# Kernel tuning notes

Hardware: AMD Instinct MI355X
Metric: run time of the kernel (lower is better)

The kernel has to match this reference:

```python
import jax, jax.numpy as jnp
import numpy as np
import math

# ---------- real Wigner 3j (Clebsch-Gordan in real spherical-harmonic basis) ----------

def _w3j_complex(l1, l2, l3):
    F = math.factorial
    tri = F(l1 + l2 - l3) * F(l1 - l2 + l3) * F(-l1 + l2 + l3) / F(l1 + l2 + l3 + 1)
    C = np.zeros((2 * l1 + 1, 2 * l2 + 1, 2 * l3 + 1))
    for m1 in range(-l1, l1 + 1):
        for m2 in range(-l2, l2 + 1):
            m3 = -m1 - m2
            if abs(m3) > l3:
                continue
            pref = (-1.0) ** (l1 - l2 - m3) * math.sqrt(
                tri * F(l1 + m1) * F(l1 - m1) * F(l2 + m2) * F(l2 - m2) * F(l3 + m3) * F(l3 - m3))
            s = 0.0
            for t in range(max(0, l2 - l3 - m1, l1 - l3 + m2),
                           min(l1 + l2 - l3, l1 - m1, l2 + m2) + 1):
                s += (-1.0) ** t / (F(t) * F(l1 + l2 - l3 - t) * F(l1 - m1 - t)
                                    * F(l2 + m2 - t) * F(l3 - l2 + m1 + t) * F(l3 - l1 - m2 + t))
            C[m1 + l1, m2 + l2, m3 + l3] = pref * s
    return C

def _U_real(l):
    # complex -> real spherical harmonic change of basis, rows indexed by real m in [-l, l]
    U = np.zeros((2 * l + 1, 2 * l + 1), dtype=complex)
    U[l, l] = 1.0
    s2 = 1.0 / math.sqrt(2.0)
    for m in range(1, l + 1):
        U[l + m, l + m] = (-1) ** m * s2
        U[l + m, l - m] = s2
        U[l - m, l - m] = 1j * s2
        U[l - m, l + m] = -1j * (-1) ** m * s2
    return U

def _w3j_real(l1, l2, l3):
    # 3j symbol is rotation invariant, so conjugating each index by U gives the real-basis 3j;
    # for even l1+l2+l3 (all paths here) the result is purely real. Frobenius norm is 1.
    Cc = _w3j_complex(l1, l2, l3)
    Cr = np.einsum('ia,jb,kc,abc->ijk', _U_real(l1), _U_real(l2), _U_real(l3), Cc)
    return np.ascontiguousarray(Cr.real.astype(np.float32))

_PATHS = [(4, 4), (4, 6), (6, 4), (6, 6)]  # CG-allowed couplings into 4e and into 6e
_CG = {(l1, l2, lo): jnp.asarray(_w3j_real(l1, l2, lo)) for lo in (4, 6) for (l1, l2) in _PATHS}
_A4 = math.sqrt(9.0 / 4.0)    # component normalization: sqrt(dim(4e) / n_paths)
_A6 = math.sqrt(13.0 / 4.0)   # component normalization: sqrt(dim(6e) / n_paths)
_K = 3                        # kernel_size
_COPIES = 4                   # upsample_factor**2


def setup_inputs() -> dict:
    key = jax.random.key(0)
    k1, k2, k3 = jax.random.split(key, 3)
    H = W = 768
    n = H * W
    return {
        'f4': jax.random.normal(k1, (n, 9), dtype=jnp.float32),
        'f6': jax.random.normal(k2, (n, 13), dtype=jnp.float32),
        'spatial_weights': jnp.ones((_K, _K), dtype=jnp.float32) / (_K * _K),
        'tp_weights': jax.random.normal(k3, (_COPIES, 8), dtype=jnp.float32),
        'H': H, 'W': W,
    }


def reference(f4, f6, spatial_weights, tp_weights, H, W):
    feats = jnp.concatenate([f4, f6], axis=-1)            # (HW, 22)
    Cch = feats.shape[-1]
    img = feats.reshape(H, W, Cch)
    pad = _K // 2
    img_p = jnp.pad(img, ((pad, pad), (pad, pad), (0, 0)), mode='edge')  # replicate padding
    # weighted 3x3 neighbor sum == depthwise conv with the shared spatial kernel
    kern = jnp.broadcast_to(spatial_weights[:, :, None, None], (_K, _K, 1, Cch)).astype(feats.dtype)
    nb = jax.lax.conv_general_dilated(
        img_p[None], kern, (1, 1), 'VALID',
        dimension_numbers=('NHWC', 'HWIO', 'NHWC'),
        feature_group_count=Cch)[0].reshape(-1, Cch)      # (HW, 22)

    x = {4: feats[:, :9], 6: feats[:, 9:]}                # center-pixel irreps
    y = {4: nb[:, :9], 6: nb[:, 9:]}                      # neighbor-aggregated irreps
    # path outputs are shared across copies; only the scalar path weights differ per copy
    t4 = jnp.stack([jnp.einsum('ijk,ni,nj->nk', _CG[(l1, l2, 4)], x[l1], y[l2]) for l1, l2 in _PATHS], 0)  # (4, HW, 9)
    t6 = jnp.stack([jnp.einsum('ijk,ni,nj->nk', _CG[(l1, l2, 6)], x[l1], y[l2]) for l1, l2 in _PATHS], 0)  # (4, HW, 13)
    out4 = _A4 * jnp.einsum('cp,pnk->nck', tp_weights[:, :4], t4)   # (HW, copies, 9)
    out6 = _A6 * jnp.einsum('cp,pnk->nck', tp_weights[:, 4:], t6)   # (HW, copies, 13)
    # per-copy [f4(9) | f6(13)] blocks concatenated along features, as in torch.cat(out_per_copy, -1)
    out = jnp.concatenate([out4, out6], axis=-1).reshape(-1, _COPIES * 22)  # (HW, 88)
    f4_size = 9 * _COPIES
    f4_out = out[:, :f4_size] + jnp.tile(f4, (1, _COPIES))   # matches torch's :36 slice + repeat residual
    f6_out = out[:, f4_size:] + jnp.tile(f6, (1, _COPIES))
    return f4_out, f6_out
```

## Files before the change

### kernel.cpp

```cpp
#include <hip/hip_runtime.h>
#include <utility>
#include <cstddef>

namespace cg {

struct FactTab { double f[24]; };
constexpr FactTab make_fact() {
  FactTab t{}; t.f[0] = 1.0;
  for (int i = 1; i < 24; ++i) t.f[i] = t.f[i-1] * (double)i;
  return t;
}
constexpr FactTab FT = make_fact();
constexpr double F(int n) { return FT.f[n]; }

constexpr double csqrt(double x) {
  if (x <= 0.0) return 0.0;
  double g = x > 1.0 ? x : 1.0;
  for (int i = 0; i < 200; ++i) {
    double ng = 0.5 * (g + x / g);
    if (ng >= g) break;
    g = ng;
  }
  return g;
}

struct T3 { double v[13][13][13]; };

constexpr T3 w3j_c(int l1, int l2, int l3) {
  T3 C{};
  const double tri = F(l1+l2-l3) * F(l1-l2+l3) * F(-l1+l2+l3) / F(l1+l2+l3+1);
  for (int m1 = -l1; m1 <= l1; ++m1) {
    for (int m2 = -l2; m2 <= l2; ++m2) {
      const int m3 = -m1 - m2;
      if (m3 < -l3 || m3 > l3) continue;
      const int e = l1 - l2 - m3;
      const double sign = (((e % 2) + 2) % 2) ? -1.0 : 1.0;
      const double pref = sign * csqrt(tri * F(l1+m1) * F(l1-m1) * F(l2+m2)
                                           * F(l2-m2) * F(l3+m3) * F(l3-m3));
      int t0 = 0;
      if (l2 - l3 - m1 > t0) t0 = l2 - l3 - m1;
      if (l1 - l3 + m2 > t0) t0 = l1 - l3 + m2;
      int t1 = l1 + l2 - l3;
      if (l1 - m1 < t1) t1 = l1 - m1;
      if (l2 + m2 < t1) t1 = l2 + m2;
      double s = 0.0;
      for (int t = t0; t <= t1; ++t) {
        const double term = 1.0 / (F(t) * F(l1+l2-l3-t) * F(l1-m1-t)
                                   * F(l2+m2-t) * F(l3-l2+m1+t) * F(l3-l1-m2+t));
        s += (t % 2) ? -term : term;
      }
      C.v[m1+l1][m2+l2][m3+l3] = pref * s;
    }
  }
  return C;
}

struct C2 { double re, im; };
constexpr C2 cmul(C2 a, C2 b) { return C2{a.re*b.re - a.im*b.im, a.re*b.im + a.im*b.re}; }

struct UCol { int n; int row[2]; C2 val[2]; };
constexpr UCol ucol(int l, int a) {
  UCol r{};
  const double s2 = csqrt(0.5);
  if (a == l) {
    r.n = 1; r.row[0] = l; r.val[0] = C2{1.0, 0.0};
  } else if (a > l) {
    const int m = a - l;
    const double sg = (m % 2) ? -1.0 : 1.0;
    r.n = 2;
    r.row[0] = l + m; r.val[0] = C2{sg * s2, 0.0};
    r.row[1] = l - m; r.val[1] = C2{0.0, -sg * s2};
  } else {
    const int m = l - a;
    r.n = 2;
    r.row[0] = l + m; r.val[0] = C2{s2, 0.0};
    r.row[1] = l - m; r.val[1] = C2{0.0, s2};
  }
  return r;
}

constexpr T3 to_real(const T3& Cc, int l1, int l2, int l3) {
  T3 R{};
  UCol U1[13]{}, U2[13]{}, U3[13]{};
  for (int a = 0; a < 2*l1+1; ++a) U1[a] = ucol(l1, a);
  for (int b = 0; b < 2*l2+1; ++b) U2[b] = ucol(l2, b);
  for (int c = 0; c < 2*l3+1; ++c) U3[c] = ucol(l3, c);
  for (int a = 0; a < 2*l1+1; ++a)
    for (int b = 0; b < 2*l2+1; ++b)
      for (int c = 0; c < 2*l3+1; ++c) {
        const double cv = Cc.v[a][b][c];
        if (cv == 0.0) continue;
        for (int ia = 0; ia < U1[a].n; ++ia)
          for (int jb = 0; jb < U2[b].n; ++jb)
            for (int kc = 0; kc < U3[c].n; ++kc) {
              C2 t = cmul(cmul(U1[a].val[ia], U2[b].val[jb]), U3[c].val[kc]);
              R.v[U1[a].row[ia]][U2[b].row[jb]][U3[c].row[kc]] += t.re * cv;
            }
      }
  return R;
}

struct Ent { short i, j, k; float v; };
constexpr int CAP = 1100;
template <int C> struct List { int n; Ent e[C]; };

constexpr List<CAP> make_list(const T3& R, int d1, int d2, int d3) {
  List<CAP> L{};
  for (int i = 0; i < d1; ++i)
    for (int j = 0; j < d2; ++j)
      for (int k = 0; k < d3; ++k) {
        const double v = R.v[i][j][k];
        if (v > 1e-10 || v < -1e-10) {
          L.e[L.n].i = (short)i; L.e[L.n].j = (short)j; L.e[L.n].k = (short)k;
          L.e[L.n].v = (float)v;
          L.n++;
        }
      }
  return L;
}

constexpr T3 CC444 = w3j_c(4,4,4);
constexpr T3 CC446 = w3j_c(4,4,6);
constexpr T3 CC464 = w3j_c(4,6,4);
constexpr T3 CC466 = w3j_c(4,6,6);
constexpr T3 CC644 = w3j_c(6,4,4);
constexpr T3 CC646 = w3j_c(6,4,6);
constexpr T3 CC664 = w3j_c(6,6,4);
constexpr T3 CC666 = w3j_c(6,6,6);

constexpr T3 CR444 = to_real(CC444, 4,4,4);
constexpr T3 CR446 = to_real(CC446, 4,4,6);
constexpr T3 CR464 = to_real(CC464, 4,6,4);
constexpr T3 CR466 = to_real(CC466, 4,6,6);
constexpr T3 CR644 = to_real(CC644, 6,4,4);
constexpr T3 CR646 = to_real(CC646, 6,4,6);
constexpr T3 CR664 = to_real(CC664, 6,6,4);
constexpr T3 CR666 = to_real(CC666, 6,6,6);

struct Tag444 { static constexpr List<CAP> L = make_list(CR444, 9, 9, 9);  };
struct Tag446 { static constexpr List<CAP> L = make_list(CR446, 9, 9, 13); };
struct Tag464 { static constexpr List<CAP> L = make_list(CR464, 9, 13, 9); };
struct Tag466 { static constexpr List<CAP> L = make_list(CR466, 9, 13, 13);};
struct Tag644 { static constexpr List<CAP> L = make_list(CR644, 13, 9, 9); };
struct Tag646 { static constexpr List<CAP> L = make_list(CR646, 13, 9, 13);};
struct Tag664 { static constexpr List<CAP> L = make_list(CR664, 13, 13, 9);};
struct Tag666 { static constexpr List<CAP> L = make_list(CR666, 13, 13, 13);};

template <class Tag, size_t... Es>
__device__ __forceinline__ void cg_apply_impl(const float* __restrict__ x,
                                              const float* __restrict__ y,
                                              float* __restrict__ acc,
                                              std::index_sequence<Es...>) {
  ((acc[(int)Tag::L.e[Es].k] +=
        Tag::L.e[Es].v * (x[(int)Tag::L.e[Es].i] * y[(int)Tag::L.e[Es].j])), ...);
}
template <class Tag>
__device__ __forceinline__ void cg_apply(const float* __restrict__ x,
                                         const float* __restrict__ y,
                                         float* __restrict__ acc) {
  cg_apply_impl<Tag>(x, y, acc, std::make_index_sequence<(size_t)Tag::L.n>{});
}

}

__global__ __launch_bounds__(256) void eq_spatial_conv_kernel(
    const float* __restrict__ f4, const float* __restrict__ f6,
    const float* __restrict__ sw, const float* __restrict__ tpw,
    const int* __restrict__ Hp, const int* __restrict__ Wp,
    float* __restrict__ out) {
  const int H = Hp[0];
  const int W = Wp[0];
  const int n = H * W;
  const int p = blockIdx.x * 256 + threadIdx.x;
  if (p >= n) return;
  const int py = p / W;
  const int px = p - py * W;

  float x4[9], x6[13];
  {
    const float* b4 = f4 + (size_t)p * 9;
#pragma unroll
    for (int c = 0; c < 9; ++c) x4[c] = b4[c];
    const float* b6 = f6 + (size_t)p * 13;
#pragma unroll
    for (int c = 0; c < 13; ++c) x6[c] = b6[c];
  }

  float w[9];
#pragma unroll
  for (int t = 0; t < 9; ++t) w[t] = sw[t];

  float y4[9], y6[13];
#pragma unroll
  for (int c = 0; c < 9; ++c) y4[c] = w[4] * x4[c];
#pragma unroll
  for (int c = 0; c < 13; ++c) y6[c] = w[4] * x6[c];

#pragma unroll
  for (int dy = -1; dy <= 1; ++dy) {
#pragma unroll
    for (int dx = -1; dx <= 1; ++dx) {
      if (dy == 0 && dx == 0) continue;
      int yy = py + dy; yy = yy < 0 ? 0 : (yy >= H ? H - 1 : yy);
      int xx = px + dx; xx = xx < 0 ? 0 : (xx >= W ? W - 1 : xx);
      const int q = yy * W + xx;
      const float wt = w[(dy + 1) * 3 + (dx + 1)];
      const float* b4 = f4 + (size_t)q * 9;
#pragma unroll
      for (int c = 0; c < 9; ++c) y4[c] += wt * b4[c];
      const float* b6 = f6 + (size_t)q * 13;
#pragma unroll
      for (int c = 0; c < 13; ++c) y6[c] += wt * b6[c];
    }
  }

  float t4[4][9];
  float t6[4][13];
#pragma unroll
  for (int pth = 0; pth < 4; ++pth) {
#pragma unroll
    for (int k = 0; k < 9; ++k) t4[pth][k] = 0.0f;
#pragma unroll
    for (int k = 0; k < 13; ++k) t6[pth][k] = 0.0f;
  }

  cg::cg_apply<cg::Tag444>(x4, y4, t4[0]);
  cg::cg_apply<cg::Tag446>(x4, y4, t6[0]);
  cg::cg_apply<cg::Tag464>(x4, y6, t4[1]);
  cg::cg_apply<cg::Tag466>(x4, y6, t6[1]);
  cg::cg_apply<cg::Tag644>(x6, y4, t4[2]);
  cg::cg_apply<cg::Tag646>(x6, y4, t6[2]);
  cg::cg_apply<cg::Tag664>(x6, y6, t4[3]);
  cg::cg_apply<cg::Tag666>(x6, y6, t6[3]);

  const float A4 = 1.5f;
  const float A6 = 1.8027756377319946f;

  float* o4base = out + (size_t)p * 36;
  float* o6base = out + (size_t)n * 36 + (size_t)p * 52;

#pragma unroll
  for (int c = 0; c < 4; ++c) {
    const float w40 = tpw[c * 8 + 0], w41 = tpw[c * 8 + 1];
    const float w42 = tpw[c * 8 + 2], w43 = tpw[c * 8 + 3];
    const float w60 = tpw[c * 8 + 4], w61 = tpw[c * 8 + 5];
    const float w62 = tpw[c * 8 + 6], w63 = tpw[c * 8 + 7];
#pragma unroll
    for (int k = 0; k < 9; ++k) {
      const float v = A4 * (w40 * t4[0][k] + w41 * t4[1][k] +
                            w42 * t4[2][k] + w43 * t4[3][k]);
      const int flat = c * 22 + k;
      if (flat < 36) o4base[flat] = v + x4[flat % 9];
      else           o6base[flat - 36] = v + x6[(flat - 36) % 13];
    }
#pragma unroll
    for (int k = 0; k < 13; ++k) {
      const float v = A6 * (w60 * t6[0][k] + w61 * t6[1][k] +
                            w62 * t6[2][k] + w63 * t6[3][k]);
      const int flat = c * 22 + 9 + k;
      if (flat < 36) o4base[flat] = v + x4[flat % 9];
      else           o6base[flat - 36] = v + x6[(flat - 36) % 13];
    }
  }
}

extern "C" void kernel_launch(void* const* d_in, const int* in_sizes, int n_in,
                              void* d_out, int out_size, void* d_ws, size_t ws_size,
                              hipStream_t stream) {
  const float* f4  = (const float*)d_in[0];
  const float* f6  = (const float*)d_in[1];
  const float* sw  = (const float*)d_in[2];
  const float* tpw = (const float*)d_in[3];
  const int*   Hp  = (const int*)d_in[4];
  const int*   Wp  = (const int*)d_in[5];
  float* out = (float*)d_out;

  const int n = in_sizes[0] / 9;
  const int blocks = (n + 255) / 256;
  eq_spatial_conv_kernel<<<dim3(blocks), dim3(256), 0, stream>>>(
      f4, f6, sw, tpw, Hp, Wp, out);
}
```

Baseline: 376.6 us.

## Tile 16x16 with LDS halo staging and vectorize output stores

Each block now handles a 16x16 spatial tile. It cooperatively loads an 18x18 halo of f4/f6 features into shared memory and reads the 3x3 depthwise neighbours from LDS instead of global memory. Outputs are gathered into registers and written with float4 stores instead of scalar strided stores. The host infers H and W by assuming a square image, which couples the grid size to the test shape. It also adds LDS pressure, roughly 30 KB per block, which may limit occupancy.

```diff
diff --git a/kernel.cpp b/kernel.cpp
--- a/kernel.cpp
+++ b/kernel.cpp
@@ -1,6 +1,7 @@
 #include <hip/hip_runtime.h>
 #include <utility>
 #include <cstddef>
+#include <cmath>
 
 namespace cg {
 
@@ -163,6 +164,12 @@
 
 }
 
+constexpr int TW = 16, TH = 16;
+constexpr int HX = TW + 2, HY = TH + 2;
+constexpr int NPIX = HX * HY;
+constexpr int N4W = NPIX * 9;
+constexpr int N6W = NPIX * 13;
+
 __global__ __launch_bounds__(256) void eq_spatial_conv_kernel(
     const float* __restrict__ f4, const float* __restrict__ f6,
     const float* __restrict__ sw, const float* __restrict__ tpw,
@@ -171,20 +178,52 @@
   const int H = Hp[0];
   const int W = Wp[0];
   const int n = H * W;
-  const int p = blockIdx.x * 256 + threadIdx.x;
-  if (p >= n) return;
-  const int py = p / W;
-  const int px = p - py * W;
+  const int tid = threadIdx.x;
+
+  const int tiles_x = (W + TW - 1) / TW;
+  const int tiley = blockIdx.x / tiles_x;
+  const int tilex = blockIdx.x - tiley * tiles_x;
+  const int bx0 = tilex * TW - 1;
+  const int by0 = tiley * TH - 1;
+
+  __shared__ float lds4[N4W];
+  __shared__ float lds6[N6W];
+
+#pragma unroll
+  for (int i = 0; i < (N4W + 255) / 256; ++i) {
+    const int w = i * 256 + tid;
+    if (w < N4W) {
+      const int pix = w / 9, ch = w - 9 * pix;
+      const int hy = pix / HX, hx = pix - HX * hy;
+      int gy = by0 + hy; gy = gy < 0 ? 0 : (gy >= H ? H - 1 : gy);
+      int gx = bx0 + hx; gx = gx < 0 ? 0 : (gx >= W ? W - 1 : gx);
+      lds4[w] = f4[(size_t)(gy * W + gx) * 9 + ch];
+    }
+  }
+#pragma unroll
+  for (int i = 0; i < (N6W + 255) / 256; ++i) {
+    const int w = i * 256 + tid;
+    if (w < N6W) {
+      const int pix = w / 13, ch = w - 13 * pix;
+      const int hy = pix / HX, hx = pix - HX * hy;
+      int gy = by0 + hy; gy = gy < 0 ? 0 : (gy >= H ? H - 1 : gy);
+      int gx = bx0 + hx; gx = gx < 0 ? 0 : (gx >= W ? W - 1 : gx);
+      lds6[w] = f6[(size_t)(gy * W + gx) * 13 + ch];
+    }
+  }
+  __syncthreads();
+
+  const int ty = tid >> 4, tx = tid & 15;
+  const int px = tilex * TW + tx;
+  const int py = tiley * TH + ty;
+  const bool valid = (px < W) && (py < H);
+  const int cpix = (ty + 1) * HX + (tx + 1);
 
   float x4[9], x6[13];
-  {
-    const float* b4 = f4 + (size_t)p * 9;
-#pragma unroll
-    for (int c = 0; c < 9; ++c) x4[c] = b4[c];
-    const float* b6 = f6 + (size_t)p * 13;
-#pragma unroll
-    for (int c = 0; c < 13; ++c) x6[c] = b6[c];
-  }
+#pragma unroll
+  for (int c = 0; c < 9; ++c) x4[c] = lds4[cpix * 9 + c];
+#pragma unroll
+  for (int c = 0; c < 13; ++c) x6[c] = lds6[cpix * 13 + c];
 
   float w[9];
 #pragma unroll
@@ -195,22 +234,17 @@
   for (int c = 0; c < 9; ++c) y4[c] = w[4] * x4[c];
 #pragma unroll
   for (int c = 0; c < 13; ++c) y6[c] = w[4] * x6[c];
-
 #pragma unroll
   for (int dy = -1; dy <= 1; ++dy) {
 #pragma unroll
     for (int dx = -1; dx <= 1; ++dx) {
       if (dy == 0 && dx == 0) continue;
-      int yy = py + dy; yy = yy < 0 ? 0 : (yy >= H ? H - 1 : yy);
-      int xx = px + dx; xx = xx < 0 ? 0 : (xx >= W ? W - 1 : xx);
-      const int q = yy * W + xx;
+      const int npix = cpix + dy * HX + dx;
       const float wt = w[(dy + 1) * 3 + (dx + 1)];
-      const float* b4 = f4 + (size_t)q * 9;
-#pragma unroll
-      for (int c = 0; c < 9; ++c) y4[c] += wt * b4[c];
-      const float* b6 = f6 + (size_t)q * 13;
-#pragma unroll
-      for (int c = 0; c < 13; ++c) y6[c] += wt * b6[c];
+#pragma unroll
+      for (int c = 0; c < 9; ++c) y4[c] += wt * lds4[npix * 9 + c];
+#pragma unroll
+      for (int c = 0; c < 13; ++c) y6[c] += wt * lds6[npix * 13 + c];
     }
   }
 
@@ -233,12 +267,13 @@
   cg::cg_apply<cg::Tag664>(x6, y6, t4[3]);
   cg::cg_apply<cg::Tag666>(x6, y6, t6[3]);
 
+  if (!valid) return;
+
   const float A4 = 1.5f;
   const float A6 = 1.8027756377319946f;
 
-  float* o4base = out + (size_t)p * 36;
-  float* o6base = out + (size_t)n * 36 + (size_t)p * 52;
-
+  float o4r[36];
+  float o6r[52];
 #pragma unroll
   for (int c = 0; c < 4; ++c) {
     const float w40 = tpw[c * 8 + 0], w41 = tpw[c * 8 + 1];
@@ -250,17 +285,35 @@
       const float v = A4 * (w40 * t4[0][k] + w41 * t4[1][k] +
                             w42 * t4[2][k] + w43 * t4[3][k]);
       const int flat = c * 22 + k;
-      if (flat < 36) o4base[flat] = v + x4[flat % 9];
-      else           o6base[flat - 36] = v + x6[(flat - 36) % 13];
+      if (flat < 36) o4r[flat] = v;
+      else           o6r[flat - 36] = v;
     }
 #pragma unroll
     for (int k = 0; k < 13; ++k) {
       const float v = A6 * (w60 * t6[0][k] + w61 * t6[1][k] +
                             w62 * t6[2][k] + w63 * t6[3][k]);
       const int flat = c * 22 + 9 + k;
-      if (flat < 36) o4base[flat] = v + x4[flat % 9];
-      else           o6base[flat - 36] = v + x6[(flat - 36) % 13];
-    }
+      if (flat < 36) o4r[flat] = v;
+      else           o6r[flat - 36] = v;
+    }
+  }
+#pragma unroll
+  for (int j = 0; j < 36; ++j) o4r[j] += x4[j % 9];
+#pragma unroll
+  for (int j = 0; j < 52; ++j) o6r[j] += x6[j % 13];
+
+  const int p = py * W + px;
+  float* __restrict__ o4p = out + (size_t)p * 36;
+  float* __restrict__ o6p = out + (size_t)n * 36 + (size_t)p * 52;
+#pragma unroll
+  for (int q = 0; q < 9; ++q) {
+    float4 v; v.x = o4r[4*q+0]; v.y = o4r[4*q+1]; v.z = o4r[4*q+2]; v.w = o4r[4*q+3];
+    reinterpret_cast<float4*>(o4p)[q] = v;
+  }
+#pragma unroll
+  for (int q = 0; q < 13; ++q) {
+    float4 v; v.x = o6r[4*q+0]; v.y = o6r[4*q+1]; v.z = o6r[4*q+2]; v.w = o6r[4*q+3];
+    reinterpret_cast<float4*>(o6p)[q] = v;
   }
 }
 
@@ -276,7 +329,9 @@
   float* out = (float*)d_out;
 
   const int n = in_sizes[0] / 9;
-  const int blocks = (n + 255) / 256;
-  eq_spatial_conv_kernel<<<dim3(blocks), dim3(256), 0, stream>>>(
+  const int Wh = (int)(sqrt((double)n) + 0.5);
+  const int Hh = n / Wh;
+  const int tiles = ((Wh + TW - 1) / TW) * ((Hh + TH - 1) / TH);
+  eq_spatial_conv_kernel<<<dim3(tiles), dim3(256), 0, stream>>>(
       f4, f6, sw, tpw, Hp, Wp, out);
 }
```

Result: faster. 367.5 us (-2.4%).

## Split depthwise conv into channel-parallel kernel and vectorize output stores

Applied to the files above, without the earlier changes.

The single per-pixel kernel becomes two kernels when workspace is large enough. The first computes the 3x3 replicate-padded depthwise conv with one thread per (pixel, channel), so neighbor loads are coalesced. The second loads the center and aggregated features and applies the CG paths, then writes outputs as float4 stores after staging them in registers. This trades an extra workspace write and read of n*22 floats, plus a second launch, for better load coalescing and wider stores. The fused fallback also gets the vectorized stores.

```diff
diff --git a/kernel.cpp b/kernel.cpp
--- a/kernel.cpp
+++ b/kernel.cpp
@@ -1,6 +1,7 @@
 #include <hip/hip_runtime.h>
 #include <utility>
 #include <cstddef>
+#include <cmath>
 
 namespace cg {
 
@@ -163,55 +164,79 @@
 
 }
 
-__global__ __launch_bounds__(256) void eq_spatial_conv_kernel(
+__global__ __launch_bounds__(256) void conv_kernel(
     const float* __restrict__ f4, const float* __restrict__ f6,
-    const float* __restrict__ sw, const float* __restrict__ tpw,
+    const float* __restrict__ sw,
+    const int* __restrict__ Hp, const int* __restrict__ Wp,
+    float* __restrict__ nb4, float* __restrict__ nb6) {
+  const int H = Hp[0], W = Wp[0];
+  const int n = H * W;
+  const int n9 = n * 9;
+  const int total = n * 22;
+  const int idx = blockIdx.x * 256 + threadIdx.x;
+  if (idx >= total) return;
+
+  float w[9];
+#pragma unroll
+  for (int t = 0; t < 9; ++t) w[t] = sw[t];
+
+  if (idx < n9) {
+    const int p = idx / 9, ch = idx - 9 * p;
+    const int py = p / W, px = p - py * W;
+    float acc = 0.0f;
+#pragma unroll
+    for (int dy = -1; dy <= 1; ++dy) {
+      int yy = py + dy; yy = yy < 0 ? 0 : (yy >= H ? H - 1 : yy);
+#pragma unroll
+      for (int dx = -1; dx <= 1; ++dx) {
+        int xx = px + dx; xx = xx < 0 ? 0 : (xx >= W ? W - 1 : xx);
+        acc += w[(dy + 1) * 3 + (dx + 1)] * f4[(size_t)(yy * W + xx) * 9 + ch];
+      }
+    }
+    nb4[idx] = acc;
+  } else {
+    const int j = idx - n9;
+    const int p = j / 13, ch = j - 13 * p;
+    const int py = p / W, px = p - py * W;
+    float acc = 0.0f;
+#pragma unroll
+    for (int dy = -1; dy <= 1; ++dy) {
+      int yy = py + dy; yy = yy < 0 ? 0 : (yy >= H ? H - 1 : yy);
+#pragma unroll
+      for (int dx = -1; dx <= 1; ++dx) {
+        int xx = px + dx; xx = xx < 0 ? 0 : (xx >= W ? W - 1 : xx);
+        acc += w[(dy + 1) * 3 + (dx + 1)] * f6[(size_t)(yy * W + xx) * 13 + ch];
+      }
+    }
+    nb6[j] = acc;
+  }
+}
+
+__global__ __launch_bounds__(256) void cgc_kernel(
+    const float* __restrict__ f4, const float* __restrict__ f6,
+    const float* __restrict__ nb4, const float* __restrict__ nb6,
+    const float* __restrict__ tpw,
     const int* __restrict__ Hp, const int* __restrict__ Wp,
     float* __restrict__ out) {
-  const int H = Hp[0];
-  const int W = Wp[0];
+  const int H = Hp[0], W = Wp[0];
   const int n = H * W;
   const int p = blockIdx.x * 256 + threadIdx.x;
   if (p >= n) return;
-  const int py = p / W;
-  const int px = p - py * W;
-
-  float x4[9], x6[13];
+
+  float x4[9], x6[13], y4[9], y6[13];
   {
-    const float* b4 = f4 + (size_t)p * 9;
-#pragma unroll
-    for (int c = 0; c < 9; ++c) x4[c] = b4[c];
-    const float* b6 = f6 + (size_t)p * 13;
-#pragma unroll
-    for (int c = 0; c < 13; ++c) x6[c] = b6[c];
-  }
-
-  float w[9];
-#pragma unroll
-  for (int t = 0; t < 9; ++t) w[t] = sw[t];
-
-  float y4[9], y6[13];
-#pragma unroll
-  for (int c = 0; c < 9; ++c) y4[c] = w[4] * x4[c];
-#pragma unroll
-  for (int c = 0; c < 13; ++c) y6[c] = w[4] * x6[c];
-
-#pragma unroll
-  for (int dy = -1; dy <= 1; ++dy) {
-#pragma unroll
-    for (int dx = -1; dx <= 1; ++dx) {
-      if (dy == 0 && dx == 0) continue;
-      int yy = py + dy; yy = yy < 0 ? 0 : (yy >= H ? H - 1 : yy);
-      int xx = px + dx; xx = xx < 0 ? 0 : (xx >= W ? W - 1 : xx);
-      const int q = yy * W + xx;
-      const float wt = w[(dy + 1) * 3 + (dx + 1)];
-      const float* b4 = f4 + (size_t)q * 9;
-#pragma unroll
-      for (int c = 0; c < 9; ++c) y4[c] += wt * b4[c];
-      const float* b6 = f6 + (size_t)q * 13;
-#pragma unroll
-      for (int c = 0; c < 13; ++c) y6[c] += wt * b6[c];
-    }
+    const float* a = f4 + (size_t)p * 9;
+#pragma unroll
+    for (int c = 0; c < 9; ++c) x4[c] = a[c];
+    const float* b = f6 + (size_t)p * 13;
+#pragma unroll
+    for (int c = 0; c < 13; ++c) x6[c] = b[c];
+    const float* cy = nb4 + (size_t)p * 9;
+#pragma unroll
+    for (int c = 0; c < 9; ++c) y4[c] = cy[c];
+    const float* d = nb6 + (size_t)p * 13;
+#pragma unroll
+    for (int c = 0; c < 13; ++c) y6[c] = d[c];
   }
 
   float t4[4][9];
@@ -236,9 +261,8 @@
   const float A4 = 1.5f;
   const float A6 = 1.8027756377319946f;
 
-  float* o4base = out + (size_t)p * 36;
-  float* o6base = out + (size_t)n * 36 + (size_t)p * 52;
-
+  float o4r[36];
+  float o6r[52];
 #pragma unroll
   for (int c = 0; c < 4; ++c) {
     const float w40 = tpw[c * 8 + 0], w41 = tpw[c * 8 + 1];
@@ -250,17 +274,146 @@
       const float v = A4 * (w40 * t4[0][k] + w41 * t4[1][k] +
                             w42 * t4[2][k] + w43 * t4[3][k]);
       const int flat = c * 22 + k;
-      if (flat < 36) o4base[flat] = v + x4[flat % 9];
-      else           o6base[flat - 36] = v + x6[(flat - 36) % 13];
+      if (flat < 36) o4r[flat] = v;
+      else           o6r[flat - 36] = v;
     }
 #pragma unroll
     for (int k = 0; k < 13; ++k) {
       const float v = A6 * (w60 * t6[0][k] + w61 * t6[1][k] +
                             w62 * t6[2][k] + w63 * t6[3][k]);
       const int flat = c * 22 + 9 + k;
-      if (flat < 36) o4base[flat] = v + x4[flat % 9];
-      else           o6base[flat - 36] = v + x6[(flat - 36) % 13];
-    }
+      if (flat < 36) o4r[flat] = v;
+      else           o6r[flat - 36] = v;
+    }
+  }
+#pragma unroll
+  for (int j = 0; j < 36; ++j) o4r[j] += x4[j % 9];
+#pragma unroll
+  for (int j = 0; j < 52; ++j) o6r[j] += x6[j % 13];
+
+  float* __restrict__ o4p = out + (size_t)p * 36;
+  float* __restrict__ o6p = out + (size_t)n * 36 + (size_t)p * 52;
+#pragma unroll
+  for (int q = 0; q < 9; ++q) {
+    float4 v; v.x = o4r[4*q+0]; v.y = o4r[4*q+1]; v.z = o4r[4*q+2]; v.w = o4r[4*q+3];
+    reinterpret_cast<float4*>(o4p)[q] = v;
+  }
+#pragma unroll
+  for (int q = 0; q < 13; ++q) {
+    float4 v; v.x = o6r[4*q+0]; v.y = o6r[4*q+1]; v.z = o6r[4*q+2]; v.w = o6r[4*q+3];
+    reinterpret_cast<float4*>(o6p)[q] = v;
+  }
+}
+
+__global__ __launch_bounds__(256) void fused_kernel(
+    const float* __restrict__ f4, const float* __restrict__ f6,
+    const float* __restrict__ sw, const float* __restrict__ tpw,
+    const int* __restrict__ Hp, const int* __restrict__ Wp,
+    float* __restrict__ out) {
+  const int H = Hp[0], W = Wp[0];
+  const int n = H * W;
+  const int p = blockIdx.x * 256 + threadIdx.x;
+  if (p >= n) return;
+  const int py = p / W;
+  const int px = p - py * W;
+
+  float x4[9], x6[13];
+  {
+    const float* b4 = f4 + (size_t)p * 9;
+#pragma unroll
+    for (int c = 0; c < 9; ++c) x4[c] = b4[c];
+    const float* b6 = f6 + (size_t)p * 13;
+#pragma unroll
+    for (int c = 0; c < 13; ++c) x6[c] = b6[c];
+  }
+  float w[9];
+#pragma unroll
+  for (int t = 0; t < 9; ++t) w[t] = sw[t];
+
+  float y4[9], y6[13];
+#pragma unroll
+  for (int c = 0; c < 9; ++c) y4[c] = w[4] * x4[c];
+#pragma unroll
+  for (int c = 0; c < 13; ++c) y6[c] = w[4] * x6[c];
+#pragma unroll
+  for (int dy = -1; dy <= 1; ++dy) {
+#pragma unroll
+    for (int dx = -1; dx <= 1; ++dx) {
+      if (dy == 0 && dx == 0) continue;
+      int yy = py + dy; yy = yy < 0 ? 0 : (yy >= H ? H - 1 : yy);
+      int xx = px + dx; xx = xx < 0 ? 0 : (xx >= W ? W - 1 : xx);
+      const int q = yy * W + xx;
+      const float wt = w[(dy + 1) * 3 + (dx + 1)];
+      const float* b4 = f4 + (size_t)q * 9;
+#pragma unroll
+      for (int c = 0; c < 9; ++c) y4[c] += wt * b4[c];
+      const float* b6 = f6 + (size_t)q * 13;
+#pragma unroll
+      for (int c = 0; c < 13; ++c) y6[c] += wt * b6[c];
+    }
+  }
+
+  float t4[4][9];
+  float t6[4][13];
+#pragma unroll
+  for (int pth = 0; pth < 4; ++pth) {
+#pragma unroll
+    for (int k = 0; k < 9; ++k) t4[pth][k] = 0.0f;
+#pragma unroll
+    for (int k = 0; k < 13; ++k) t6[pth][k] = 0.0f;
+  }
+  cg::cg_apply<cg::Tag444>(x4, y4, t4[0]);
+  cg::cg_apply<cg::Tag446>(x4, y4, t6[0]);
+  cg::cg_apply<cg::Tag464>(x4, y6, t4[1]);
+  cg::cg_apply<cg::Tag466>(x4, y6, t6[1]);
+  cg::cg_apply<cg::Tag644>(x6, y4, t4[2]);
+  cg::cg_apply<cg::Tag646>(x6, y4, t6[2]);
+  cg::cg_apply<cg::Tag664>(x6, y6, t4[3]);
+  cg::cg_apply<cg::Tag666>(x6, y6, t6[3]);
+
+  const float A4 = 1.5f;
+  const float A6 = 1.8027756377319946f;
+  float o4r[36];
+  float o6r[52];
+#pragma unroll
+  for (int c = 0; c < 4; ++c) {
+    const float w40 = tpw[c * 8 + 0], w41 = tpw[c * 8 + 1];
+    const float w42 = tpw[c * 8 + 2], w43 = tpw[c * 8 + 3];
+    const float w60 = tpw[c * 8 + 4], w61 = tpw[c * 8 + 5];
+    const float w62 = tpw[c * 8 + 6], w63 = tpw[c * 8 + 7];
+#pragma unroll
+    for (int k = 0; k < 9; ++k) {
+      const float v = A4 * (w40 * t4[0][k] + w41 * t4[1][k] +
+                            w42 * t4[2][k] + w43 * t4[3][k]);
+      const int flat = c * 22 + k;
+      if (flat < 36) o4r[flat] = v;
+      else           o6r[flat - 36] = v;
+    }
+#pragma unroll
+    for (int k = 0; k < 13; ++k) {
+      const float v = A6 * (w60 * t6[0][k] + w61 * t6[1][k] +
+                            w62 * t6[2][k] + w63 * t6[3][k]);
+      const int flat = c * 22 + 9 + k;
+      if (flat < 36) o4r[flat] = v;
+      else           o6r[flat - 36] = v;
+    }
+  }
+#pragma unroll
+  for (int j = 0; j < 36; ++j) o4r[j] += x4[j % 9];
+#pragma unroll
+  for (int j = 0; j < 52; ++j) o6r[j] += x6[j % 13];
+
+  float* __restrict__ o4p = out + (size_t)p * 36;
+  float* __restrict__ o6p = out + (size_t)n * 36 + (size_t)p * 52;
+#pragma unroll
+  for (int q = 0; q < 9; ++q) {
+    float4 v; v.x = o4r[4*q+0]; v.y = o4r[4*q+1]; v.z = o4r[4*q+2]; v.w = o4r[4*q+3];
+    reinterpret_cast<float4*>(o4p)[q] = v;
+  }
+#pragma unroll
+  for (int q = 0; q < 13; ++q) {
+    float4 v; v.x = o6r[4*q+0]; v.y = o6r[4*q+1]; v.z = o6r[4*q+2]; v.w = o6r[4*q+3];
+    reinterpret_cast<float4*>(o6p)[q] = v;
   }
 }
 
@@ -276,7 +429,20 @@
   float* out = (float*)d_out;
 
   const int n = in_sizes[0] / 9;
-  const int blocks = (n + 255) / 256;
-  eq_spatial_conv_kernel<<<dim3(blocks), dim3(256), 0, stream>>>(
-      f4, f6, sw, tpw, Hp, Wp, out);
-}
+  const size_t need = (size_t)n * 22 * sizeof(float);
+
+  if (ws_size >= need) {
+    float* nb4 = (float*)d_ws;
+    float* nb6 = nb4 + (size_t)n * 9;
+    const int convBlocks = (n * 22 + 255) / 256;
+    conv_kernel<<<dim3(convBlocks), dim3(256), 0, stream>>>(
+        f4, f6, sw, Hp, Wp, nb4, nb6);
+    const int cgBlocks = (n + 255) / 256;
+    cgc_kernel<<<dim3(cgBlocks), dim3(256), 0, stream>>>(
+        f4, f6, nb4, nb6, tpw, Hp, Wp, out);
+  } else {
+    const int blocks = (n + 255) / 256;
+    fused_kernel<<<dim3(blocks), dim3(256), 0, stream>>>(
+        f4, f6, sw, tpw, Hp, Wp, out);
+  }
+}
```

Result: no change. 373.0 us (-0.9%).

## Split CG output paths across two thread roles and vectorize feature loads

Applied to the files above, without the earlier changes.

Each pixel is now handled by two threads: the first half of each block computes the four paths into the l=4 output and the second half the four paths into the l=6 output. Center and neighbor features are read with unaligned 4-wide vector loads, and the clamped neighbor indices are precomputed. This cuts per-thread CG arithmetic and register pressure so more waves can be resident. The cost is that both threads repeat the 3x3 neighbor gather, doubling those loads, and the two halves of a wave do unequal amounts of work.

```diff
diff --git a/kernel.cpp b/kernel.cpp
--- a/kernel.cpp
+++ b/kernel.cpp
@@ -1,6 +1,7 @@
 #include <hip/hip_runtime.h>
 #include <utility>
 #include <cstddef>
+#include <cmath>
 
 namespace cg {
 
@@ -163,27 +164,37 @@
 
 }
 
-__global__ __launch_bounds__(256) void eq_spatial_conv_kernel(
+typedef float v4u __attribute__((ext_vector_type(4), aligned(4)));
+
+__global__ __launch_bounds__(256) void fused_split_kernel(
     const float* __restrict__ f4, const float* __restrict__ f6,
     const float* __restrict__ sw, const float* __restrict__ tpw,
     const int* __restrict__ Hp, const int* __restrict__ Wp,
     float* __restrict__ out) {
-  const int H = Hp[0];
-  const int W = Wp[0];
+  const int H = Hp[0], W = Wp[0];
   const int n = H * W;
-  const int p = blockIdx.x * 256 + threadIdx.x;
+  const int tid = threadIdx.x;
+  const bool role6 = tid >= 128;
+  const int p = blockIdx.x * 128 + (tid & 127);
   if (p >= n) return;
   const int py = p / W;
   const int px = p - py * W;
 
   float x4[9], x6[13];
   {
-    const float* b4 = f4 + (size_t)p * 9;
-#pragma unroll
-    for (int c = 0; c < 9; ++c) x4[c] = b4[c];
-    const float* b6 = f6 + (size_t)p * 13;
-#pragma unroll
-    for (int c = 0; c < 13; ++c) x6[c] = b6[c];
+    const float* a = f4 + (size_t)p * 9;
+    v4u v0 = *reinterpret_cast<const v4u*>(a);
+    v4u v1 = *reinterpret_cast<const v4u*>(a + 4);
+#pragma unroll
+    for (int c = 0; c < 4; ++c) { x4[c] = v0[c]; x4[c + 4] = v1[c]; }
+    x4[8] = a[8];
+    const float* b = f6 + (size_t)p * 13;
+    v4u u0 = *reinterpret_cast<const v4u*>(b);
+    v4u u1 = *reinterpret_cast<const v4u*>(b + 4);
+    v4u u2 = *reinterpret_cast<const v4u*>(b + 8);
+#pragma unroll
+    for (int c = 0; c < 4; ++c) { x6[c] = u0[c]; x6[c + 4] = u1[c]; x6[c + 8] = u2[c]; }
+    x6[12] = b[12];
   }
 
   float w[9];
@@ -196,70 +207,84 @@
 #pragma unroll
   for (int c = 0; c < 13; ++c) y6[c] = w[4] * x6[c];
 
-#pragma unroll
-  for (int dy = -1; dy <= 1; ++dy) {
-#pragma unroll
-    for (int dx = -1; dx <= 1; ++dx) {
-      if (dy == 0 && dx == 0) continue;
-      int yy = py + dy; yy = yy < 0 ? 0 : (yy >= H ? H - 1 : yy);
-      int xx = px + dx; xx = xx < 0 ? 0 : (xx >= W ? W - 1 : xx);
-      const int q = yy * W + xx;
-      const float wt = w[(dy + 1) * 3 + (dx + 1)];
-      const float* b4 = f4 + (size_t)q * 9;
-#pragma unroll
-      for (int c = 0; c < 9; ++c) y4[c] += wt * b4[c];
-      const float* b6 = f6 + (size_t)q * 13;
-#pragma unroll
-      for (int c = 0; c < 13; ++c) y6[c] += wt * b6[c];
+  const int xm1 = px > 0 ? px - 1 : 0;
+  const int xp1 = px < W - 1 ? px + 1 : W - 1;
+  const int rm1 = (py > 0 ? py - 1 : 0) * W;
+  const int r0  = py * W;
+  const int rp1 = (py < H - 1 ? py + 1 : H - 1) * W;
+
+  const int qs[8] = { rm1 + xm1, rm1 + px, rm1 + xp1,
+                      r0 + xm1,             r0 + xp1,
+                      rp1 + xm1, rp1 + px, rp1 + xp1 };
+  const float ws[8] = { w[0], w[1], w[2], w[3], w[5], w[6], w[7], w[8] };
+
+#pragma unroll
+  for (int t = 0; t < 8; ++t) {
+    const int q = qs[t];
+    const float wt = ws[t];
+    const float* b4 = f4 + (size_t)q * 9;
+    v4u a0 = *reinterpret_cast<const v4u*>(b4);
+    v4u a1 = *reinterpret_cast<const v4u*>(b4 + 4);
+#pragma unroll
+    for (int c = 0; c < 4; ++c) { y4[c] += wt * a0[c]; y4[c + 4] += wt * a1[c]; }
+    y4[8] += wt * b4[8];
+    const float* b6 = f6 + (size_t)q * 13;
+    v4u c0 = *reinterpret_cast<const v4u*>(b6);
+    v4u c1 = *reinterpret_cast<const v4u*>(b6 + 4);
+    v4u c2 = *reinterpret_cast<const v4u*>(b6 + 8);
+#pragma unroll
+    for (int c = 0; c < 4; ++c) {
+      y6[c] += wt * c0[c]; y6[c + 4] += wt * c1[c]; y6[c + 8] += wt * c2[c];
     }
-  }
-
-  float t4[4][9];
-  float t6[4][13];
-#pragma unroll
-  for (int pth = 0; pth < 4; ++pth) {
-#pragma unroll
-    for (int k = 0; k < 9; ++k) t4[pth][k] = 0.0f;
-#pragma unroll
-    for (int k = 0; k < 13; ++k) t6[pth][k] = 0.0f;
-  }
-
-  cg::cg_apply<cg::Tag444>(x4, y4, t4[0]);
-  cg::cg_apply<cg::Tag446>(x4, y4, t6[0]);
-  cg::cg_apply<cg::Tag464>(x4, y6, t4[1]);
-  cg::cg_apply<cg::Tag466>(x4, y6, t6[1]);
-  cg::cg_apply<cg::Tag644>(x6, y4, t4[2]);
-  cg::cg_apply<cg::Tag646>(x6, y4, t6[2]);
-  cg::cg_apply<cg::Tag664>(x6, y6, t4[3]);
-  cg::cg_apply<cg::Tag666>(x6, y6, t6[3]);
-
-  const float A4 = 1.5f;
-  const float A6 = 1.8027756377319946f;
-
-  float* o4base = out + (size_t)p * 36;
-  float* o6base = out + (size_t)n * 36 + (size_t)p * 52;
-
-#pragma unroll
-  for (int c = 0; c < 4; ++c) {
-    const float w40 = tpw[c * 8 + 0], w41 = tpw[c * 8 + 1];
-    const float w42 = tpw[c * 8 + 2], w43 = tpw[c * 8 + 3];
-    const float w60 = tpw[c * 8 + 4], w61 = tpw[c * 8 + 5];
-    const float w62 = tpw[c * 8 + 6], w63 = tpw[c * 8 + 7];
-#pragma unroll
-    for (int k = 0; k < 9; ++k) {
-      const float v = A4 * (w40 * t4[0][k] + w41 * t4[1][k] +
-                            w42 * t4[2][k] + w43 * t4[3][k]);
-      const int flat = c * 22 + k;
-      if (flat < 36) o4base[flat] = v + x4[flat % 9];
-      else           o6base[flat - 36] = v + x6[(flat - 36) % 13];
+    y6[12] += wt * b6[12];
+  }
+
+  float* __restrict__ o4p = out + (size_t)p * 36;
+  float* __restrict__ o6p = out + (size_t)n * 36 + (size_t)p * 52;
+
+  if (!role6) {
+    float t0[9], t1[9], t2[9], t3[9];
+#pragma unroll
+    for (int k = 0; k < 9; ++k) { t0[k] = t1[k] = t2[k] = t3[k] = 0.0f; }
+    cg::cg_apply<cg::Tag444>(x4, y4, t0);
+    cg::cg_apply<cg::Tag464>(x4, y6, t1);
+    cg::cg_apply<cg::Tag644>(x6, y4, t2);
+    cg::cg_apply<cg::Tag664>(x6, y6, t3);
+
+    const float A4 = 1.5f;
+#pragma unroll
+    for (int c = 0; c < 4; ++c) {
+      const float w0 = tpw[c * 8 + 0], w1 = tpw[c * 8 + 1];
+      const float w2 = tpw[c * 8 + 2], w3 = tpw[c * 8 + 3];
+#pragma unroll
+      for (int k = 0; k < 9; ++k) {
+        const int flat = c * 22 + k;
+        float v = A4 * (w0 * t0[k] + w1 * t1[k] + w2 * t2[k] + w3 * t3[k]);
+        if (flat < 36) { v += x4[flat % 9];         o4p[flat] = v; }
+        else           { v += x6[(flat - 36) % 13]; o6p[flat - 36] = v; }
+      }
     }
-#pragma unroll
-    for (int k = 0; k < 13; ++k) {
-      const float v = A6 * (w60 * t6[0][k] + w61 * t6[1][k] +
-                            w62 * t6[2][k] + w63 * t6[3][k]);
-      const int flat = c * 22 + 9 + k;
-      if (flat < 36) o4base[flat] = v + x4[flat % 9];
-      else           o6base[flat - 36] = v + x6[(flat - 36) % 13];
+  } else {
+    float s0[13], s1[13], s2[13], s3[13];
+#pragma unroll
+    for (int k = 0; k < 13; ++k) { s0[k] = s1[k] = s2[k] = s3[k] = 0.0f; }
+    cg::cg_apply<cg::Tag446>(x4, y4, s0);
+    cg::cg_apply<cg::Tag466>(x4, y6, s1);
+    cg::cg_apply<cg::Tag646>(x6, y4, s2);
+    cg::cg_apply<cg::Tag666>(x6, y6, s3);
+
+    const float A6 = 1.8027756377319946f;
+#pragma unroll
+    for (int c = 0; c < 4; ++c) {
+      const float w0 = tpw[c * 8 + 4], w1 = tpw[c * 8 + 5];
+      const float w2 = tpw[c * 8 + 6], w3 = tpw[c * 8 + 7];
+#pragma unroll
+      for (int k = 0; k < 13; ++k) {
+        const int flat = c * 22 + 9 + k;
+        float v = A6 * (w0 * s0[k] + w1 * s1[k] + w2 * s2[k] + w3 * s3[k]);
+        if (flat < 36) { v += x4[flat % 9];         o4p[flat] = v; }
+        else           { v += x6[(flat - 36) % 13]; o6p[flat - 36] = v; }
+      }
     }
   }
 }
@@ -276,7 +301,7 @@
   float* out = (float*)d_out;
 
   const int n = in_sizes[0] / 9;
-  const int blocks = (n + 255) / 256;
-  eq_spatial_conv_kernel<<<dim3(blocks), dim3(256), 0, stream>>>(
+  const int blocks = (n + 127) / 128;
+  fused_split_kernel<<<dim3(blocks), dim3(256), 0, stream>>>(
       f4, f6, sw, tpw, Hp, Wp, out);
 }
```

Measured after the change: 376.8 us. No clear change (+0.1%).
